# Performance work log

Hardware: AMD Instinct MI355X
Metric: run time of the kernel (lower is better)

Reference implementation:

```python
import jax, jax.numpy as jnp
import numpy as np

B, H, W = 32, 32, 32
C_CNN, C_EFF, HID = 512, 1280, 512


def conv1x1(x, w, b):
    # x: [B, Cin, H, W], w: [Cout, Cin], b: [Cout]
    return jnp.einsum('bchw,oc->bohw', x, w) + b[None, :, None, None]


def setup_inputs() -> dict:
    key = jax.random.key(0)
    ks = jax.random.split(key, 12)
    s = 0.02  # small init scale keeps softmax logits well-conditioned
    return {
        'cnn_features': jax.random.normal(ks[0], (B, C_CNN, H, W), jnp.float32),
        'efficient_features': jax.random.normal(ks[1], (B, C_EFF, H, W), jnp.float32),
        'W_cnn': jax.random.normal(ks[2], (HID, C_CNN), jnp.float32) * s,
        'b_cnn': jnp.zeros((HID,), jnp.float32),
        'W_eff': jax.random.normal(ks[3], (HID, C_EFF), jnp.float32) * s,
        'b_eff': jnp.zeros((HID,), jnp.float32),
        'W_q': jax.random.normal(ks[4], (HID, HID), jnp.float32) * s,
        'b_q': jnp.zeros((HID,), jnp.float32),
        'W_k': jax.random.normal(ks[5], (HID, HID), jnp.float32) * s,
        'b_k': jnp.zeros((HID,), jnp.float32),
        'W_v': jax.random.normal(ks[6], (HID, HID), jnp.float32) * s,
        'b_v': jnp.zeros((HID,), jnp.float32),
        'gamma': jnp.asarray([0.1], jnp.float32),
    }


def reference(cnn_features, efficient_features, W_cnn, b_cnn, W_eff, b_eff,
              W_q, b_q, W_k, b_k, W_v, b_v, gamma):
    cnn_proj = conv1x1(cnn_features, W_cnn, b_cnn)          # [B, HID, H, W]
    eff_proj = conv1x1(efficient_features, W_eff, b_eff)    # [B, HID, H, W]
    b, c, h, w = cnn_proj.shape
    n = h * w
    # 1x1 conv QKV projections then flatten spatial dims into tokens
    q = conv1x1(cnn_proj, W_q, b_q).reshape(b, c, n).transpose(0, 2, 1)  # [B, N, C]
    k = conv1x1(eff_proj, W_k, b_k).reshape(b, c, n)                     # [B, C, N]
    v = conv1x1(eff_proj, W_v, b_v).reshape(b, c, n).transpose(0, 2, 1)  # [B, N, C]
    attn = jax.nn.softmax(jnp.einsum('bnc,bcm->bnm', q, k), axis=-1)     # [B, N, N] (unscaled, as in source)
    out = jnp.einsum('bnm,bmc->bnc', attn, v)                            # [B, N, C]
    out = out.transpose(0, 2, 1).reshape(b, c, h, w)
    return gamma[0] * out + cnn_proj
```

## Files before the change

### kernel.cpp

```cpp
#include <hip/hip_runtime.h>
#include <hip/hip_bf16.h>
#include <cstdint>


typedef __hip_bfloat16 bf16;
typedef __bf16 bf16x8 __attribute__((ext_vector_type(8)));
typedef float f32x4 __attribute__((ext_vector_type(4)));

#define NB   32
#define NTOK 1024
#define NHID 512
#define CEFF 1280

struct W5 { const float *s0, *s1, *s2, *s3, *s4; };
#define W5_N0 (NHID*NHID)
#define W5_N1 (W5_N0 + NHID*CEFF)
#define W5_N2 (W5_N1 + NHID*NHID)
#define W5_N3 (W5_N2 + NHID*NHID)
#define W5_N4 (W5_N3 + NHID*NHID)
__global__ __launch_bounds__(256) void convert_weights_kernel(W5 w, bf16* __restrict__ dst) {
    int i = blockIdx.x * 256 + threadIdx.x;
    float v;
    if      (i < W5_N0) v = w.s0[i];
    else if (i < W5_N1) v = w.s1[i - W5_N0];
    else if (i < W5_N2) v = w.s2[i - W5_N1];
    else if (i < W5_N3) v = w.s3[i - W5_N2];
    else if (i < W5_N4) v = w.s4[i - W5_N3];
    else return;
    dst[i] = __float2bfloat16(v);
}

__global__ __launch_bounds__(256) void transpose_to_bf16_kernel(const float* __restrict__ in,
                                                                bf16* __restrict__ out,
                                                                int C, int N) {
    __shared__ float tile[32][33];
    const int n0 = blockIdx.x * 32, c0 = blockIdx.y * 32, b = blockIdx.z;
    in  += (size_t)b * C * N;
    out += (size_t)b * N * C;
    const int tx = threadIdx.x, ty = threadIdx.y;
    #pragma unroll
    for (int i = ty; i < 32; i += 8)
        tile[i][tx] = in[(size_t)(c0 + i) * N + n0 + tx];
    __syncthreads();
    #pragma unroll
    for (int i = ty; i < 32; i += 8)
        out[(size_t)(n0 + i) * C + c0 + tx] = __float2bfloat16(tile[tx][i]);
}

__global__ __launch_bounds__(256) void gemm_bt_kernel(
    const bf16* __restrict__ A, long long aStride, int lda,
    const bf16* __restrict__ Bt, long long bStride, int ldb,
    int K,
    const float* __restrict__ bias,
    float* __restrict__ outF, long long fStride, int ldf,
    const float* __restrict__ resid, const float* __restrict__ gammaPtr,
    const float* __restrict__ rowInv,
    bf16* __restrict__ outHt, long long htStride, int ldht,
    bf16* __restrict__ outHn, long long hnStride, int ldhn, int doExp)
{
    __shared__ __bf16 lA[128 * 32];
    __shared__ __bf16 lB[128 * 32];

    const int tid  = threadIdx.x;
    const int wave = tid >> 6;
    const int lane = tid & 63;
    const int bz   = blockIdx.z;
    const int m0   = blockIdx.y * 128;
    const int n0   = blockIdx.x * 128;

    const bf16* Ab = A  + (size_t)bz * aStride;
    const bf16* Bb = Bt + (size_t)bz * bStride;

    const int wm = wave >> 1, wn = wave & 1;
    const int lrow = lane & 15, quad = lane >> 4;

    f32x4 acc[4][4];
    #pragma unroll
    for (int i = 0; i < 4; i++)
        #pragma unroll
        for (int j = 0; j < 4; j++)
            acc[i][j] = (f32x4){0.f, 0.f, 0.f, 0.f};

    const int rowl = lane >> 2;
    const int qsw  = (lane & 3) ^ ((lane >> 3) & 3);
    const bf16* gA0 = Ab + (size_t)(m0 +      wave * 16 + rowl) * lda + qsw * 8;
    const bf16* gA1 = Ab + (size_t)(m0 + 64 + wave * 16 + rowl) * lda + qsw * 8;
    const bf16* gB0 = Bb + (size_t)(n0 +      wave * 16 + rowl) * ldb + qsw * 8;
    const bf16* gB1 = Bb + (size_t)(n0 + 64 + wave * 16 + rowl) * ldb + qsw * 8;
    __bf16* lA0 = &lA[(wave * 64) * 8];
    __bf16* lA1 = &lA[(256 + wave * 64) * 8];
    __bf16* lB0 = &lB[(wave * 64) * 8];
    __bf16* lB1 = &lB[(256 + wave * 64) * 8];

    const int sw = quad ^ ((lrow >> 1) & 3);
    int aoff[4], boff[4];
    #pragma unroll
    for (int mt = 0; mt < 4; mt++) aoff[mt] = ((wm * 4 + mt) * 64 + lrow * 4 + sw) * 8;
    #pragma unroll
    for (int nt = 0; nt < 4; nt++) boff[nt] = ((wn * 4 + nt) * 64 + lrow * 4 + sw) * 8;

    for (int k0 = 0; k0 < K; k0 += 32) {
        __builtin_amdgcn_global_load_lds((const __attribute__((address_space(1))) void*)(gA0 + k0),
                                         (__attribute__((address_space(3))) void*)lA0, 16, 0, 0);
        __builtin_amdgcn_global_load_lds((const __attribute__((address_space(1))) void*)(gA1 + k0),
                                         (__attribute__((address_space(3))) void*)lA1, 16, 0, 0);
        __builtin_amdgcn_global_load_lds((const __attribute__((address_space(1))) void*)(gB0 + k0),
                                         (__attribute__((address_space(3))) void*)lB0, 16, 0, 0);
        __builtin_amdgcn_global_load_lds((const __attribute__((address_space(1))) void*)(gB1 + k0),
                                         (__attribute__((address_space(3))) void*)lB1, 16, 0, 0);
        __syncthreads();

        bf16x8 af[4], bfr[4];
        #pragma unroll
        for (int mt = 0; mt < 4; mt++) af[mt]  = *(const bf16x8*)&lA[aoff[mt]];
        #pragma unroll
        for (int nt = 0; nt < 4; nt++) bfr[nt] = *(const bf16x8*)&lB[boff[nt]];
        #pragma unroll
        for (int mt = 0; mt < 4; mt++)
            #pragma unroll
            for (int nt = 0; nt < 4; nt++)
                acc[mt][nt] = __builtin_amdgcn_mfma_f32_16x16x32_bf16(af[mt], bfr[nt], acc[mt][nt], 0, 0, 0);
        __syncthreads();
    }

    const float gscale = gammaPtr ? gammaPtr[0] : 1.0f;
    #pragma unroll
    for (int mt = 0; mt < 4; mt++) {
        const int mbase = m0 + wm * 64 + mt * 16 + quad * 4;
        float bv[4];
        #pragma unroll
        for (int r = 0; r < 4; r++) bv[r] = bias ? bias[mbase + r] : 0.f;
        #pragma unroll
        for (int nt = 0; nt < 4; nt++) {
            const int n = n0 + wn * 64 + nt * 16 + lrow;
            float v[4];
            #pragma unroll
            for (int r = 0; r < 4; r++) v[r] = acc[mt][nt][r] + bv[r];
            if (outF) {
                float* p = outF + (size_t)bz * fStride;
                const float* rp = resid ? resid + (size_t)bz * fStride : nullptr;
                const float rinv = rowInv ? rowInv[(size_t)bz * NTOK + n] : 1.0f;
                #pragma unroll
                for (int r = 0; r < 4; r++) {
                    size_t idx = (size_t)(mbase + r) * ldf + n;
                    p[idx] = gscale * v[r] * rinv + (rp ? rp[idx] : 0.f);
                }
            }
            if (outHt) {
                union { bf16 h[4]; unsigned long long u; } pk;
                #pragma unroll
                for (int r = 0; r < 4; r++) pk.h[r] = __float2bfloat16(v[r]);
                *(unsigned long long*)&outHt[(size_t)bz * htStride + (size_t)n * ldht + mbase] = pk.u;
            }
            if (outHn) {
                bf16* p = outHn + (size_t)bz * hnStride;
                #pragma unroll
                for (int r = 0; r < 4; r++) {
                    float sv = doExp ? __expf(v[r]) : v[r];
                    p[(size_t)(mbase + r) * ldhn + n] = __float2bfloat16(sv);
                }
            }
        }
    }
}

__global__ __launch_bounds__(256) void rowinv_kernel(const bf16* __restrict__ P,
                                                     float* __restrict__ inv) {
    const bf16* row = P + (size_t)blockIdx.x * NTOK;
    const int t = threadIdx.x;
    ushort4 u = *(const ushort4*)(row + t * 4);
    union { unsigned int ui; float f; } c0, c1, c2, c3;
    c0.ui = (unsigned)u.x << 16; c1.ui = (unsigned)u.y << 16;
    c2.ui = (unsigned)u.z << 16; c3.ui = (unsigned)u.w << 16;
    float s = c0.f + c1.f + c2.f + c3.f;
    #pragma unroll
    for (int off = 32; off >= 1; off >>= 1) s += __shfl_xor(s, off, 64);
    __shared__ float red[4];
    if ((t & 63) == 0) red[t >> 6] = s;
    __syncthreads();
    if (t == 0) inv[blockIdx.x] = 1.0f / (red[0] + red[1] + red[2] + red[3]);
}

extern "C" void kernel_launch(void* const* d_in, const int* in_sizes, int n_in,
                              void* d_out, int out_size, void* d_ws, size_t ws_size,
                              hipStream_t stream) {
    const float* x_cnn = (const float*)d_in[0];
    const float* x_eff = (const float*)d_in[1];
    const float* W_cnn = (const float*)d_in[2];
    const float* b_cnn = (const float*)d_in[3];
    const float* W_eff = (const float*)d_in[4];
    const float* b_eff = (const float*)d_in[5];
    const float* W_q   = (const float*)d_in[6];
    const float* b_q   = (const float*)d_in[7];
    const float* W_k   = (const float*)d_in[8];
    const float* b_k   = (const float*)d_in[9];
    const float* W_v   = (const float*)d_in[10];
    const float* b_v   = (const float*)d_in[11];
    const float* gamma = (const float*)d_in[12];
    float* out = (float*)d_out;

    uint8_t* ws = (uint8_t*)d_ws;
    size_t off = 0;
    auto alloc = [&](size_t bytes) -> uint8_t* {
        uint8_t* p = ws + off;
        off = (off + bytes + 255) & ~(size_t)255;
        return p;
    };

    bf16* Wall  = (bf16*)alloc((size_t)W5_N4 * 2);
    bf16* Wc_h  = Wall;
    bf16* We_h  = Wall + W5_N0;
    bf16* Wq_h  = Wall + W5_N1;
    bf16* Wk_h  = Wall + W5_N2;
    bf16* Wv_h  = Wall + W5_N3;
    bf16* Xc_t  = (bf16*)alloc((size_t)NB * NTOK * NHID * 2);
    bf16* Xe_t  = (bf16*)alloc((size_t)NB * NTOK * CEFF * 2);
    float* cnn_proj = (float*)alloc((size_t)NB * NHID * NTOK * 4);
    bf16* projc_t = (bf16*)alloc((size_t)NB * NTOK * NHID * 2);
    bf16* proje_t = (bf16*)alloc((size_t)NB * NTOK * NHID * 2);
    float* rowInv = (float*)alloc((size_t)NB * NTOK * 4);

    const size_t pBytesPer = (size_t)NTOK * NTOK * 2;
    int G = 32;
    while (G > 1 && off + (size_t)G * pBytesPer + 256 > ws_size) G >>= 1;
    bf16* P = (bf16*)alloc((size_t)G * pBytesPer);

    bf16* q_t  = Xc_t;
    bf16* k_t  = Xe_t;
    bf16* v_nt = Xe_t + (size_t)NB * NTOK * NHID;

    {
        W5 w{W_cnn, W_eff, W_q, W_k, W_v};
        convert_weights_kernel<<<(W5_N4 + 255) / 256, 256, 0, stream>>>(w, Wall);
    }

    transpose_to_bf16_kernel<<<dim3(NTOK / 32, NHID / 32, NB), dim3(32, 8), 0, stream>>>(x_cnn, Xc_t, NHID, NTOK);
    transpose_to_bf16_kernel<<<dim3(NTOK / 32, CEFF / 32, NB), dim3(32, 8), 0, stream>>>(x_eff, Xe_t, CEFF, NTOK);

    auto gemm = [&](dim3 grid,
                    const bf16* A, long long aS, int lda,
                    const bf16* Bt, long long bS, int ldb, int K,
                    const float* bias,
                    float* oF, long long fS, int ldf, const float* resid, const float* gp,
                    const float* rInv,
                    bf16* oHt, long long htS, int ldht,
                    bf16* oHn, long long hnS, int ldhn, int doExp) {
        gemm_bt_kernel<<<grid, 256, 0, stream>>>(A, aS, lda, Bt, bS, ldb, K, bias,
                                                 oF, fS, ldf, resid, gp, rInv,
                                                 oHt, htS, ldht, oHn, hnS, ldhn, doExp);
    };

    const long long sNC = (long long)NTOK * NHID;
    const long long sCN = (long long)NHID * NTOK;

    gemm(dim3(8, 4, NB), Wc_h, 0, NHID, Xc_t, sNC, NHID, NHID, b_cnn,
         cnn_proj, sCN, NTOK, nullptr, nullptr, nullptr,
         projc_t, sNC, NHID, nullptr, 0, 0, 0);
    gemm(dim3(8, 4, NB), We_h, 0, CEFF, Xe_t, (long long)NTOK * CEFF, CEFF, CEFF, b_eff,
         nullptr, 0, 0, nullptr, nullptr, nullptr,
         proje_t, sNC, NHID, nullptr, 0, 0, 0);
    gemm(dim3(8, 4, NB), Wq_h, 0, NHID, projc_t, sNC, NHID, NHID, b_q,
         nullptr, 0, 0, nullptr, nullptr, nullptr,
         q_t, sNC, NHID, nullptr, 0, 0, 0);
    gemm(dim3(8, 4, NB), Wk_h, 0, NHID, proje_t, sNC, NHID, NHID, b_k,
         nullptr, 0, 0, nullptr, nullptr, nullptr,
         k_t, sNC, NHID, nullptr, 0, 0, 0);
    gemm(dim3(8, 4, NB), Wv_h, 0, NHID, proje_t, sNC, NHID, NHID, b_v,
         nullptr, 0, 0, nullptr, nullptr, nullptr,
         nullptr, 0, 0, v_nt, sCN, NTOK, 0);

    for (int g = 0; g < NB; g += G) {
        gemm(dim3(8, 8, G), q_t + (size_t)g * sNC, sNC, NHID,
             k_t + (size_t)g * sNC, sNC, NHID, NHID, nullptr,
             nullptr, 0, 0, nullptr, nullptr, nullptr,
             nullptr, 0, 0,
             P, (long long)NTOK * NTOK, NTOK, 1);
        rowinv_kernel<<<G * NTOK, 256, 0, stream>>>(P, rowInv);
        gemm(dim3(8, 4, G), v_nt + (size_t)g * sCN, sCN, NTOK,
             P, (long long)NTOK * NTOK, NTOK, NTOK, nullptr,
             out + (size_t)g * sCN, sCN, NTOK, cnn_proj + (size_t)g * sCN, gamma, rowInv,
             nullptr, 0, 0, nullptr, 0, 0, 0);
    }
}
```

Before: 819.5 us.

## Fold projection weights into QKV, fuse row-sum into exp GEMM, swizzle grid

Precomputes composed weights Wq·Wcnn and [Wk;Wv]·Weff (plus fused biases), so the attention inputs come straight from the raw features. This removes the intermediate projection GEMMs, and K and V are produced by a single GEMM. The softmax row sum is accumulated inside the exp GEMM epilogue with atomics, which removes the separate rowinv kernel. The residual is stored as bf16, P reuses the Xe_t buffer, and blocks are remapped so each batch's tiles are scheduled together for cache reuse. Composing the weights in bf16 and keeping the residual in bf16 both add rounding error.

```diff
diff --git a/kernel.cpp b/kernel.cpp
--- a/kernel.cpp
+++ b/kernel.cpp
@@ -11,23 +11,13 @@
 #define NTOK 1024
 #define NHID 512
 #define CEFF 1280
-
-struct W5 { const float *s0, *s1, *s2, *s3, *s4; };
-#define W5_N0 (NHID*NHID)
-#define W5_N1 (W5_N0 + NHID*CEFF)
-#define W5_N2 (W5_N1 + NHID*NHID)
-#define W5_N3 (W5_N2 + NHID*NHID)
-#define W5_N4 (W5_N3 + NHID*NHID)
-__global__ __launch_bounds__(256) void convert_weights_kernel(W5 w, bf16* __restrict__ dst) {
+#define WSZ  (NHID*NHID)
+
+struct W4 { const float* s[4]; };
+__global__ __launch_bounds__(256) void convert_w4_kernel(W4 w, bf16* __restrict__ dst) {
     int i = blockIdx.x * 256 + threadIdx.x;
-    float v;
-    if      (i < W5_N0) v = w.s0[i];
-    else if (i < W5_N1) v = w.s1[i - W5_N0];
-    else if (i < W5_N2) v = w.s2[i - W5_N1];
-    else if (i < W5_N3) v = w.s3[i - W5_N2];
-    else if (i < W5_N4) v = w.s4[i - W5_N3];
-    else return;
-    dst[i] = __float2bfloat16(v);
+    int sel = i >> 18, off = i & (WSZ - 1);
+    dst[i] = __float2bfloat16(w.s[sel][off]);
 }
 
 __global__ __launch_bounds__(256) void transpose_to_bf16_kernel(const float* __restrict__ in,
@@ -47,26 +37,50 @@
         out[(size_t)(n0 + i) * C + c0 + tx] = __float2bfloat16(tile[tx][i]);
 }
 
+__global__ __launch_bounds__(256) void bias_fuse_kernel(
+    const float* __restrict__ Wq, const float* __restrict__ Wk, const float* __restrict__ Wv,
+    const float* __restrict__ bc, const float* __restrict__ be,
+    const float* __restrict__ bq, const float* __restrict__ bk, const float* __restrict__ bv,
+    float* __restrict__ bqc, float* __restrict__ bkv) {
+    const int r = blockIdx.x, t = threadIdx.x;
+    const float* Wrow; const float* vin; float badd; float* dst;
+    if (r < 512)       { Wrow = Wq + (size_t)r * 512;          vin = bc; badd = bq[r];        dst = bqc + r; }
+    else if (r < 1024) { Wrow = Wk + (size_t)(r - 512) * 512;  vin = be; badd = bk[r - 512];  dst = bkv + (r - 512); }
+    else               { Wrow = Wv + (size_t)(r - 1024) * 512; vin = be; badd = bv[r - 1024]; dst = bkv + (r - 512); }
+    float s = Wrow[t] * vin[t] + Wrow[t + 256] * vin[t + 256];
+    #pragma unroll
+    for (int off = 32; off >= 1; off >>= 1) s += __shfl_xor(s, off, 64);
+    __shared__ float red[4];
+    if ((t & 63) == 0) red[t >> 6] = s;
+    __syncthreads();
+    if (t == 0) dst[0] = red[0] + red[1] + red[2] + red[3] + badd;
+}
+
 __global__ __launch_bounds__(256) void gemm_bt_kernel(
     const bf16* __restrict__ A, long long aStride, int lda,
     const bf16* __restrict__ Bt, long long bStride, int ldb,
-    int K,
+    int K, int swiz,
     const float* __restrict__ bias,
     float* __restrict__ outF, long long fStride, int ldf,
-    const float* __restrict__ resid, const float* __restrict__ gammaPtr,
-    const float* __restrict__ rowInv,
-    bf16* __restrict__ outHt, long long htStride, int ldht,
-    bf16* __restrict__ outHn, long long hnStride, int ldhn, int doExp)
+    const bf16* __restrict__ residH, const float* __restrict__ gammaPtr,
+    const float* __restrict__ rsumIn,
+    float* __restrict__ rsumOut,
+    bf16* __restrict__ outHt, long long htStride, int ldht, int htMax,
+    bf16* __restrict__ outHn, long long hnStride, int ldhn, int hnBase, int doExp)
 {
     __shared__ __bf16 lA[128 * 32];
     __shared__ __bf16 lB[128 * 32];
+    __shared__ float lrs[128];
 
     const int tid  = threadIdx.x;
     const int wave = tid >> 6;
     const int lane = tid & 63;
-    const int bz   = blockIdx.z;
-    const int m0   = blockIdx.y * 128;
-    const int n0   = blockIdx.x * 128;
+
+    int bx, by, bz;
+    if (swiz) { bx = (int)blockIdx.y & 7; by = (int)blockIdx.y >> 3; bz = (int)blockIdx.z * 8 + (int)blockIdx.x; }
+    else      { bx = (int)blockIdx.x;     by = (int)blockIdx.y;      bz = (int)blockIdx.z; }
+    const int m0 = by * 128;
+    const int n0 = bx * 128;
 
     const bf16* Ab = A  + (size_t)bz * aStride;
     const bf16* Bb = Bt + (size_t)bz * bStride;
@@ -124,6 +138,13 @@
     }
 
     const float gscale = gammaPtr ? gammaPtr[0] : 1.0f;
+    float rs[4][4];
+    if (rsumOut)
+        #pragma unroll
+        for (int mt = 0; mt < 4; mt++)
+            #pragma unroll
+            for (int r = 0; r < 4; r++) rs[mt][r] = 0.f;
+
     #pragma unroll
     for (int mt = 0; mt < 4; mt++) {
         const int mbase = m0 + wm * 64 + mt * 16 + quad * 4;
@@ -135,50 +156,60 @@
             const int n = n0 + wn * 64 + nt * 16 + lrow;
             float v[4];
             #pragma unroll
-            for (int r = 0; r < 4; r++) v[r] = acc[mt][nt][r] + bv[r];
+            for (int r = 0; r < 4; r++) {
+                v[r] = acc[mt][nt][r] + bv[r];
+                if (doExp) v[r] = __expf(v[r]);
+                if (rsumOut) rs[mt][r] += v[r];
+            }
             if (outF) {
                 float* p = outF + (size_t)bz * fStride;
-                const float* rp = resid ? resid + (size_t)bz * fStride : nullptr;
-                const float rinv = rowInv ? rowInv[(size_t)bz * NTOK + n] : 1.0f;
+                const bf16* rp = residH + (size_t)bz * fStride;
+                const float rinv = rsumIn ? 1.0f / rsumIn[(size_t)bz * NTOK + n] : 1.0f;
                 #pragma unroll
                 for (int r = 0; r < 4; r++) {
                     size_t idx = (size_t)(mbase + r) * ldf + n;
-                    p[idx] = gscale * v[r] * rinv + (rp ? rp[idx] : 0.f);
+                    p[idx] = gscale * v[r] * rinv + __bfloat162float(rp[idx]);
                 }
             }
-            if (outHt) {
+            if (outHt && mbase < htMax) {
                 union { bf16 h[4]; unsigned long long u; } pk;
                 #pragma unroll
                 for (int r = 0; r < 4; r++) pk.h[r] = __float2bfloat16(v[r]);
                 *(unsigned long long*)&outHt[(size_t)bz * htStride + (size_t)n * ldht + mbase] = pk.u;
             }
-            if (outHn) {
+            if (outHn && mbase >= hnBase) {
                 bf16* p = outHn + (size_t)bz * hnStride;
                 #pragma unroll
-                for (int r = 0; r < 4; r++) {
-                    float sv = doExp ? __expf(v[r]) : v[r];
-                    p[(size_t)(mbase + r) * ldhn + n] = __float2bfloat16(sv);
-                }
+                for (int r = 0; r < 4; r++)
+                    p[(size_t)(mbase - hnBase + r) * ldhn + n] = __float2bfloat16(v[r]);
             }
         }
     }
-}
-
-__global__ __launch_bounds__(256) void rowinv_kernel(const bf16* __restrict__ P,
-                                                     float* __restrict__ inv) {
-    const bf16* row = P + (size_t)blockIdx.x * NTOK;
-    const int t = threadIdx.x;
-    ushort4 u = *(const ushort4*)(row + t * 4);
-    union { unsigned int ui; float f; } c0, c1, c2, c3;
-    c0.ui = (unsigned)u.x << 16; c1.ui = (unsigned)u.y << 16;
-    c2.ui = (unsigned)u.z << 16; c3.ui = (unsigned)u.w << 16;
-    float s = c0.f + c1.f + c2.f + c3.f;
-    #pragma unroll
-    for (int off = 32; off >= 1; off >>= 1) s += __shfl_xor(s, off, 64);
-    __shared__ float red[4];
-    if ((t & 63) == 0) red[t >> 6] = s;
-    __syncthreads();
-    if (t == 0) inv[blockIdx.x] = 1.0f / (red[0] + red[1] + red[2] + red[3]);
+
+    if (rsumOut) {
+        #pragma unroll
+        for (int mt = 0; mt < 4; mt++)
+            #pragma unroll
+            for (int r = 0; r < 4; r++) {
+                float s = rs[mt][r];
+                s += __shfl_xor(s, 1, 64);
+                s += __shfl_xor(s, 2, 64);
+                s += __shfl_xor(s, 4, 64);
+                s += __shfl_xor(s, 8, 64);
+                rs[mt][r] = s;
+            }
+        if (tid < 128) lrs[tid] = 0.f;
+        __syncthreads();
+        if (lrow == 0) {
+            #pragma unroll
+            for (int mt = 0; mt < 4; mt++)
+                #pragma unroll
+                for (int r = 0; r < 4; r++)
+                    atomicAdd(&lrs[wm * 64 + mt * 16 + quad * 4 + r], rs[mt][r]);
+        }
+        __syncthreads();
+        if (tid < 128) atomicAdd(&rsumOut[(size_t)bz * NTOK + m0 + tid], lrs[tid]);
+    }
 }
 
 extern "C" void kernel_launch(void* const* d_in, const int* in_sizes, int n_in,
@@ -207,78 +238,78 @@
         return p;
     };
 
-    bf16* Wall  = (bf16*)alloc((size_t)W5_N4 * 2);
+    bf16* Wall  = (bf16*)alloc((size_t)4 * WSZ * 2);
     bf16* Wc_h  = Wall;
-    bf16* We_h  = Wall + W5_N0;
-    bf16* Wq_h  = Wall + W5_N1;
-    bf16* Wk_h  = Wall + W5_N2;
-    bf16* Wv_h  = Wall + W5_N3;
+    bf16* Wq_h  = Wall + WSZ;
+    bf16* Wkv_h = Wall + 2 * (size_t)WSZ;
+    bf16* Wct   = (bf16*)alloc((size_t)NHID * NHID * 2);
+    bf16* Wet   = (bf16*)alloc((size_t)CEFF * NHID * 2);
+    bf16* Wqc   = (bf16*)alloc((size_t)NHID * NHID * 2);
+    bf16* Wkve  = (bf16*)alloc((size_t)1024 * CEFF * 2);
+    float* bqc  = (float*)alloc(NHID * 4);
+    float* bkv  = (float*)alloc(1024 * 4);
+    float* rowSum = (float*)alloc((size_t)NB * NTOK * 4);
     bf16* Xc_t  = (bf16*)alloc((size_t)NB * NTOK * NHID * 2);
     bf16* Xe_t  = (bf16*)alloc((size_t)NB * NTOK * CEFF * 2);
-    float* cnn_proj = (float*)alloc((size_t)NB * NHID * NTOK * 4);
-    bf16* projc_t = (bf16*)alloc((size_t)NB * NTOK * NHID * 2);
-    bf16* proje_t = (bf16*)alloc((size_t)NB * NTOK * NHID * 2);
-    float* rowInv = (float*)alloc((size_t)NB * NTOK * 4);
-
-    const size_t pBytesPer = (size_t)NTOK * NTOK * 2;
-    int G = 32;
-    while (G > 1 && off + (size_t)G * pBytesPer + 256 > ws_size) G >>= 1;
-    bf16* P = (bf16*)alloc((size_t)G * pBytesPer);
-
-    bf16* q_t  = Xc_t;
-    bf16* k_t  = Xe_t;
-    bf16* v_nt = Xe_t + (size_t)NB * NTOK * NHID;
+    bf16* resid = (bf16*)alloc((size_t)NB * NHID * NTOK * 2);
+    bf16* q_t   = (bf16*)alloc((size_t)NB * NTOK * NHID * 2);
+    bf16* k_t   = (bf16*)alloc((size_t)NB * NTOK * NHID * 2);
+    bf16* v_nt  = (bf16*)alloc((size_t)NB * NHID * NTOK * 2);
+    bf16* P     = Xe_t;
 
     {
-        W5 w{W_cnn, W_eff, W_q, W_k, W_v};
-        convert_weights_kernel<<<(W5_N4 + 255) / 256, 256, 0, stream>>>(w, Wall);
+        W4 w; w.s[0] = W_cnn; w.s[1] = W_q; w.s[2] = W_k; w.s[3] = W_v;
+        convert_w4_kernel<<<4 * WSZ / 256, 256, 0, stream>>>(w, Wall);
     }
+    transpose_to_bf16_kernel<<<dim3(NHID / 32, NHID / 32, 1), dim3(32, 8), 0, stream>>>(W_cnn, Wct, NHID, NHID);
+    transpose_to_bf16_kernel<<<dim3(CEFF / 32, NHID / 32, 1), dim3(32, 8), 0, stream>>>(W_eff, Wet, NHID, CEFF);
 
     transpose_to_bf16_kernel<<<dim3(NTOK / 32, NHID / 32, NB), dim3(32, 8), 0, stream>>>(x_cnn, Xc_t, NHID, NTOK);
     transpose_to_bf16_kernel<<<dim3(NTOK / 32, CEFF / 32, NB), dim3(32, 8), 0, stream>>>(x_eff, Xe_t, CEFF, NTOK);
 
-    auto gemm = [&](dim3 grid,
+    bias_fuse_kernel<<<1536, 256, 0, stream>>>(W_q, W_k, W_v, b_cnn, b_eff, b_q, b_k, b_v, bqc, bkv);
+
+    hipMemsetAsync(rowSum, 0, (size_t)NB * NTOK * 4, stream);
+
+    auto gemm = [&](dim3 grid, int swiz,
                     const bf16* A, long long aS, int lda,
                     const bf16* Bt, long long bS, int ldb, int K,
                     const float* bias,
-                    float* oF, long long fS, int ldf, const float* resid, const float* gp,
-                    const float* rInv,
-                    bf16* oHt, long long htS, int ldht,
-                    bf16* oHn, long long hnS, int ldhn, int doExp) {
-        gemm_bt_kernel<<<grid, 256, 0, stream>>>(A, aS, lda, Bt, bS, ldb, K, bias,
-                                                 oF, fS, ldf, resid, gp, rInv,
-                                                 oHt, htS, ldht, oHn, hnS, ldhn, doExp);
+                    float* oF, long long fS, int ldf, const bf16* rH, const float* gp,
+                    const float* rIn, float* rOut,
+                    bf16* oHt, long long htS, int ldht, int htMax,
+                    bf16* oHn, long long hnS, int ldhn, int hnBase, int doExp) {
+        gemm_bt_kernel<<<grid, 256, 0, stream>>>(A, aS, lda, Bt, bS, ldb, K, swiz, bias,
+                                                 oF, fS, ldf, rH, gp, rIn, rOut,
+                                                 oHt, htS, ldht, htMax, oHn, hnS, ldhn, hnBase, doExp);
     };
 
     const long long sNC = (long long)NTOK * NHID;
     const long long sCN = (long long)NHID * NTOK;
-
-    gemm(dim3(8, 4, NB), Wc_h, 0, NHID, Xc_t, sNC, NHID, NHID, b_cnn,
-         cnn_proj, sCN, NTOK, nullptr, nullptr, nullptr,
-         projc_t, sNC, NHID, nullptr, 0, 0, 0);
-    gemm(dim3(8, 4, NB), We_h, 0, CEFF, Xe_t, (long long)NTOK * CEFF, CEFF, CEFF, b_eff,
-         nullptr, 0, 0, nullptr, nullptr, nullptr,
-         proje_t, sNC, NHID, nullptr, 0, 0, 0);
-    gemm(dim3(8, 4, NB), Wq_h, 0, NHID, projc_t, sNC, NHID, NHID, b_q,
-         nullptr, 0, 0, nullptr, nullptr, nullptr,
-         q_t, sNC, NHID, nullptr, 0, 0, 0);
-    gemm(dim3(8, 4, NB), Wk_h, 0, NHID, proje_t, sNC, NHID, NHID, b_k,
-         nullptr, 0, 0, nullptr, nullptr, nullptr,
-         k_t, sNC, NHID, nullptr, 0, 0, 0);
-    gemm(dim3(8, 4, NB), Wv_h, 0, NHID, proje_t, sNC, NHID, NHID, b_v,
-         nullptr, 0, 0, nullptr, nullptr, nullptr,
-         nullptr, 0, 0, v_nt, sCN, NTOK, 0);
-
-    for (int g = 0; g < NB; g += G) {
-        gemm(dim3(8, 8, G), q_t + (size_t)g * sNC, sNC, NHID,
-             k_t + (size_t)g * sNC, sNC, NHID, NHID, nullptr,
-             nullptr, 0, 0, nullptr, nullptr, nullptr,
-             nullptr, 0, 0,
-             P, (long long)NTOK * NTOK, NTOK, 1);
-        rowinv_kernel<<<G * NTOK, 256, 0, stream>>>(P, rowInv);
-        gemm(dim3(8, 4, G), v_nt + (size_t)g * sCN, sCN, NTOK,
-             P, (long long)NTOK * NTOK, NTOK, NTOK, nullptr,
-             out + (size_t)g * sCN, sCN, NTOK, cnn_proj + (size_t)g * sCN, gamma, rowInv,
-             nullptr, 0, 0, nullptr, 0, 0, 0);
-    }
-}
+    const long long sNE = (long long)NTOK * CEFF;
+    const long long sPP = (long long)NTOK * NTOK;
+
+    gemm(dim3(4, 4, 1), 0, Wq_h, 0, NHID, Wct, 0, NHID, NHID, nullptr,
+         nullptr, 0, 0, nullptr, nullptr, nullptr, nullptr,
+         nullptr, 0, 0, 0, Wqc, 0, NHID, 0, 0);
+    gemm(dim3(10, 8, 1), 0, Wkv_h, 0, NHID, Wet, 0, NHID, NHID, nullptr,
+         nullptr, 0, 0, nullptr, nullptr, nullptr, nullptr,
+         nullptr, 0, 0, 0, Wkve, 0, CEFF, 0, 0);
+
+    gemm(dim3(8, 32, 4), 1, Wc_h, 0, NHID, Xc_t, sNC, NHID, NHID, b_cnn,
+         nullptr, 0, 0, nullptr, nullptr, nullptr, nullptr,
+         nullptr, 0, 0, 0, resid, sCN, NTOK, 0, 0);
+    gemm(dim3(8, 32, 4), 1, Wqc, 0, NHID, Xc_t, sNC, NHID, NHID, bqc,
+         nullptr, 0, 0, nullptr, nullptr, nullptr, nullptr,
+         q_t, sNC, NHID, 1 << 30, nullptr, 0, 0, 0, 0);
+    gemm(dim3(8, 64, 4), 1, Wkve, 0, CEFF, Xe_t, sNE, CEFF, CEFF, bkv,
+         nullptr, 0, 0, nullptr, nullptr, nullptr, nullptr,
+         k_t, sNC, NHID, NHID,
+         v_nt, sCN, NTOK, NHID, 0);
+    gemm(dim3(8, 64, 4), 1, q_t, sNC, NHID, k_t, sNC, NHID, NHID, nullptr,
+         nullptr, 0, 0, nullptr, nullptr, nullptr, rowSum,
+         nullptr, 0, 0, 0, P, sPP, NTOK, 0, 1);
+    gemm(dim3(8, 32, 4), 1, v_nt, sCN, NTOK, P, sPP, NTOK, NTOK, nullptr,
+         out, sCN, NTOK, resid, gamma, rowSum, nullptr,
+         nullptr, 0, 0, 0, nullptr, 0, 0, 0, 0);
+}
```

New measurement: 790.5 us. -3.6%, faster.
